# Performance work log

Measured on AMD Instinct MI355X. Metric: run time of the kernel, lower is better.

## Reference

```python
import jax, jax.numpy as jnp
import numpy as np

N_NODES = 100000
N_EDGES = 1600000
IN_FEAT = 128
HIDDEN = 128
N_CLASSES = 40


def setup_inputs() -> dict:
    key = jax.random.key(0)
    k1, k2, k3, k4 = jax.random.split(key, 4)
    x = jax.random.normal(k1, (N_NODES, IN_FEAT), dtype=jnp.float32)
    edge_index = jax.random.randint(k2, (2, N_EDGES), 0, N_NODES, dtype=jnp.int64)
    W1 = jax.random.normal(k3, (IN_FEAT, HIDDEN), dtype=jnp.float32) * (1.0 / np.sqrt(IN_FEAT))
    b1 = jnp.zeros((HIDDEN,), dtype=jnp.float32)
    W2 = jax.random.normal(k4, (HIDDEN, N_CLASSES), dtype=jnp.float32) * (1.0 / np.sqrt(HIDDEN))
    b2 = jnp.zeros((N_CLASSES,), dtype=jnp.float32)
    return {"x": x, "edge_index": edge_index, "W1": W1, "b1": b1, "W2": W2, "b2": b2}


def _gcn_conv(x, row, col, W, b, n_nodes):
    # x: [N, F_in] -> [N, F_out]; GCNConv: lin -> gather -> deg-norm -> scatter-add -> +bias
    h = x @ W  # dense transform first (PyG GCNConv order)
    # add self-loops
    loops = jnp.arange(n_nodes, dtype=row.dtype)
    row = jnp.concatenate([row, loops])
    col = jnp.concatenate([col, loops])
    # symmetric degree normalization: deg computed on destination (col)
    deg = jax.ops.segment_sum(jnp.ones_like(col, dtype=h.dtype), col, num_segments=n_nodes)
    dis = jnp.where(deg > 0, jax.lax.rsqrt(deg), 0.0)
    norm = dis[row] * dis[col]  # [E+N]
    msg = h[row] * norm[:, None]  # [E+N, F_out] gather + scale
    out = jax.ops.segment_sum(msg, col, num_segments=n_nodes)  # scatter-add
    return out + b


def reference(x, edge_index, W1, b1, W2, b2):
    row, col = edge_index[0], edge_index[1]
    n = x.shape[0]
    h = _gcn_conv(x, row, col, W1, b1, n)
    h = jax.nn.relu(h)
    # dropout p=0 / eval mode -> identity
    h = _gcn_conv(h, row, col, W2, b2, n)
    return jax.nn.log_softmax(h, axis=1)
```

## Files before the change

kernel.cpp:

```cpp
#include <hip/hip_runtime.h>
#include <hip/hip_bf16.h>
#include <math.h>

typedef unsigned short u16x8 __attribute__((ext_vector_type(8)));
typedef short s16x8 __attribute__((ext_vector_type(8)));
typedef float f32x4 __attribute__((ext_vector_type(4)));

#define BIN_TILE 4096
#define BCAP 8192

__device__ __forceinline__ float bf2f(unsigned int u) {
    union { unsigned int i; float f; } x;
    x.i = u << 16;
    return x.f;
}
__device__ __forceinline__ unsigned short f2bf(float f) {
    __hip_bfloat16 h = __float2bfloat16(f);
    return *reinterpret_cast<unsigned short*>(&h);
}

__global__ void bin_kernel(const int* __restrict__ row, const int* __restrict__ col,
                           int* __restrict__ bcnt, unsigned* __restrict__ tmp, int E, int NB) {
    __shared__ unsigned hist[512];
    int tid = threadIdx.x;
    int base = blockIdx.x * BIN_TILE;
    for (int i = tid; i < NB; i += 256) hist[i] = 0;
    __syncthreads();
#pragma unroll
    for (int i = 0; i < BIN_TILE / 256; i++) {
        int e = base + tid + i * 256;
        if (e < E) atomicAdd(&hist[col[e] >> 8], 1u);
    }
    __syncthreads();
    for (int i = tid; i < NB; i += 256) {
        unsigned h = hist[i];
        hist[i] = h ? (unsigned)atomicAdd(&bcnt[i], (int)h) : 0u;
    }
    __syncthreads();
#pragma unroll
    for (int i = 0; i < BIN_TILE / 256; i++) {
        int e = base + tid + i * 256;
        if (e < E) {
            int c = col[e], r = row[e];
            unsigned p = atomicAdd(&hist[c >> 8], 1u);
            tmp[(size_t)(c >> 8) * BCAP + p] = (unsigned)r | ((unsigned)(c & 255) << 20);
        }
    }
}

__global__ void bucket_kernel(const unsigned* __restrict__ tmp, const int* __restrict__ bcnt,
                              int* __restrict__ cnt, int* __restrict__ offs,
                              float* __restrict__ dis, int* __restrict__ csr, int N, int NB) {
    __shared__ int cntS[256], curS[256], sA[256], sB[256];
    int b = blockIdx.x;
    int tid = threadIdx.x;
    size_t tbase = (size_t)b * BCAP;

    cntS[tid] = 0;
    int partial = 0;
    if (tid < b) partial += bcnt[tid];
    if (tid + 256 < b) partial += bcnt[tid + 256];
    sA[tid] = partial;
    __syncthreads();
    for (int s = 128; s > 0; s >>= 1) {
        if (tid < s) sA[tid] += sA[tid + s];
        __syncthreads();
    }
    int start = sA[0];
    int ecnt = bcnt[b];

    for (int i = tid; i < ecnt; i += 256)
        atomicAdd(&cntS[(tmp[tbase + i] >> 20) & 255], 1);
    __syncthreads();
    int myCnt = cntS[tid];
    sA[tid] = myCnt;
    __syncthreads();
    int* src = sA;
    int* dst = sB;
    for (int off = 1; off < 256; off <<= 1) {
        dst[tid] = src[tid] + ((tid >= off) ? src[tid - off] : 0);
        __syncthreads();
        int* t = src; src = dst; dst = t;
    }
    int excl = src[tid] - myCnt;
    int node = (b << 8) + tid;
    if (node < N) {
        cnt[node] = myCnt;
        offs[node] = start + excl;
        dis[node] = rsqrtf((float)myCnt + 1.0f);
    }
    curS[tid] = excl;
    __syncthreads();
    for (int i = tid; i < ecnt; i += 256) {
        unsigned u = tmp[tbase + i];
        int cl = (u >> 20) & 255;
        int p = atomicAdd(&curS[cl], 1);
        csr[start + p] = (int)(u & 0xFFFFFu);
    }
}

__global__ void scale_cvt_kernel(const float* __restrict__ x, const float* __restrict__ dis,
                                 unsigned short* __restrict__ xbs, int N) {
    long idx = (long)blockIdx.x * blockDim.x + threadIdx.x;
    long total8 = (long)(N + 1) * 16;
    if (idx >= total8) return;
    int i = (int)(idx >> 4);
    u16x8 o;
    if (i >= N) {
#pragma unroll
        for (int k = 0; k < 8; k++) o[k] = 0;
    } else {
        float d = dis[i];
        float4 a = ((const float4*)x)[2 * idx];
        float4 b = ((const float4*)x)[2 * idx + 1];
        o[0] = f2bf(d * a.x); o[1] = f2bf(d * a.y); o[2] = f2bf(d * a.z); o[3] = f2bf(d * a.w);
        o[4] = f2bf(d * b.x); o[5] = f2bf(d * b.y); o[6] = f2bf(d * b.z); o[7] = f2bf(d * b.w);
    }
    ((u16x8*)xbs)[idx] = o;
}

__global__ void prep_kernel(const float* __restrict__ W1, const float* __restrict__ W2,
                            unsigned short* __restrict__ w1p, unsigned short* __restrict__ w2p,
                            unsigned* __restrict__ h2z) {
    int bid = blockIdx.x, tid = threadIdx.x;
    if (bid < 8) {
        int t = bid * 256 + tid;
        int lane = t & 63, fc = t >> 6;
        int ct = fc >> 2, kc = fc & 3;
        int n = ct * 16 + (lane & 15);
        int k0 = kc * 32 + (lane >> 4) * 8;
        u16x8 o;
#pragma unroll
        for (int j = 0; j < 8; j++) o[j] = f2bf(W1[(size_t)(k0 + j) * 128 + n]);
        ((u16x8*)w1p)[t] = o;
    } else if (bid < 11) {
        int t = (bid - 8) * 256 + tid;
        int lane = t & 63, fc = t >> 6;
        int ct = fc >> 2, kc = fc & 3;
        int n = ct * 16 + (lane & 15);
        int k0 = kc * 32 + (lane >> 4) * 8;
        u16x8 o;
#pragma unroll
        for (int j = 0; j < 8; j++) o[j] = (n < 40) ? f2bf(W2[(size_t)(k0 + j) * 40 + n]) : (unsigned short)0;
        ((u16x8*)w2p)[t] = o;
    } else {
        if (tid < 32) h2z[tid] = 0;
    }
}

__global__ void gather1_kernel(const unsigned short* __restrict__ xbs, const int* __restrict__ offs,
                               const int* __restrict__ cnt, const int* __restrict__ csr,
                               const float* __restrict__ dis, unsigned short* __restrict__ xa, int N) {
    int node = blockIdx.x * 4 + (threadIdx.x >> 6);
    int lane = threadIdx.x & 63;
    if (node >= N) return;
    int off = offs[node], dg = cnt[node];
    int g = lane >> 4, c = lane & 15;
    const u16x8* XB = (const u16x8*)xbs;
    float acc[8] = {};
    int s0 = (g      < dg) ? csr[off + g]      : N;
    int s1 = (g + 4  < dg) ? csr[off + g + 4]  : N;
    int s2 = (g + 8  < dg) ? csr[off + g + 8]  : N;
    int s3 = (g + 12 < dg) ? csr[off + g + 12] : N;
    for (int j = 0; j < dg; j += 16) {
        int jb = j + 16;
        int t0 = (jb + g      < dg) ? csr[off + jb + g]      : N;
        int t1 = (jb + g + 4  < dg) ? csr[off + jb + g + 4]  : N;
        int t2 = (jb + g + 8  < dg) ? csr[off + jb + g + 8]  : N;
        int t3 = (jb + g + 12 < dg) ? csr[off + jb + g + 12] : N;
        u16x8 v0 = XB[(size_t)s0 * 16 + c];
        u16x8 v1 = XB[(size_t)s1 * 16 + c];
        u16x8 v2 = XB[(size_t)s2 * 16 + c];
        u16x8 v3 = XB[(size_t)s3 * 16 + c];
#pragma unroll
        for (int k = 0; k < 8; k++)
            acc[k] += (bf2f(v0[k]) + bf2f(v1[k])) + (bf2f(v2[k]) + bf2f(v3[k]));
        s0 = t0; s1 = t1; s2 = t2; s3 = t3;
    }
#pragma unroll
    for (int k = 0; k < 8; k++) {
        acc[k] += __shfl_xor(acc[k], 16);
        acc[k] += __shfl_xor(acc[k], 32);
    }
    float dc = dis[node];
    u16x8 xv = XB[(size_t)node * 16 + c];
    if (lane < 16) {
        u16x8 o;
#pragma unroll
        for (int k = 0; k < 8; k++) o[k] = f2bf(dc * (acc[k] + bf2f(xv[k])));
        ((u16x8*)xa)[(size_t)node * 16 + c] = o;
    }
}

__global__ __launch_bounds__(256) void mlp_kernel(const unsigned short* __restrict__ xa,
                                                  const unsigned short* __restrict__ w1p,
                                                  const unsigned short* __restrict__ w2p,
                                                  const float* __restrict__ b1,
                                                  const float* __restrict__ dis,
                                                  unsigned short* __restrict__ h2s, int N) {
    __shared__ unsigned short a1s[64][136];
    int wv = threadIdx.x >> 6;
    int l = threadIdx.x & 63;
    int row16 = l & 15, kg = l >> 4;
    int n0 = blockIdx.x * 64;
    int rbase = n0 + wv * 16;

    f32x4 acc[8];
#pragma unroll
    for (int ct = 0; ct < 8; ct++) acc[ct] = (f32x4)0.f;
    int r = rbase + row16;
    int rc = (r < N) ? r : (N - 1);
#pragma unroll
    for (int kc = 0; kc < 4; kc++) {
        s16x8 af = *(const s16x8*)(xa + (size_t)rc * 128 + kc * 32 + kg * 8);
#pragma unroll
        for (int ct = 0; ct < 8; ct++) {
            s16x8 bf = *(const s16x8*)(w1p + (size_t)((ct * 4 + kc) * 64 + l) * 8);
            acc[ct] = __builtin_amdgcn_mfma_f32_16x16x32_bf16(af, bf, acc[ct], 0, 0, 0);
        }
    }
#pragma unroll
    for (int ct = 0; ct < 8; ct++) {
        float bb = b1[ct * 16 + row16];
#pragma unroll
        for (int v = 0; v < 4; v++)
            a1s[wv * 16 + kg * 4 + v][ct * 16 + row16] = f2bf(fmaxf(acc[ct][v] + bb, 0.f));
    }
    __syncthreads();

    f32x4 acc2[3];
#pragma unroll
    for (int ct = 0; ct < 3; ct++) acc2[ct] = (f32x4)0.f;
#pragma unroll
    for (int kc = 0; kc < 4; kc++) {
        s16x8 af = *(const s16x8*)&a1s[wv * 16 + row16][kc * 32 + kg * 8];
#pragma unroll
        for (int ct = 0; ct < 3; ct++) {
            s16x8 bf = *(const s16x8*)(w2p + (size_t)((ct * 4 + kc) * 64 + l) * 8);
            acc2[ct] = __builtin_amdgcn_mfma_f32_16x16x32_bf16(af, bf, acc2[ct], 0, 0, 0);
        }
    }
#pragma unroll
    for (int v = 0; v < 4; v++) {
        int rr = rbase + kg * 4 + v;
        if (rr < N) {
            float d = dis[rr];
#pragma unroll
            for (int ct = 0; ct < 3; ct++)
                h2s[(size_t)rr * 64 + ct * 16 + row16] = f2bf(d * acc2[ct][v]);
        }
    }
}

__global__ void gather2_kernel(const unsigned short* __restrict__ h2s, const int* __restrict__ offs,
                               const int* __restrict__ cnt, const int* __restrict__ csr,
                               const float* __restrict__ dis, const float* __restrict__ b2,
                               float* __restrict__ out, int N) {
    int node = blockIdx.x * 4 + (threadIdx.x >> 6);
    int lane = threadIdx.x & 63;
    if (node >= N) return;
    int off = offs[node], dg = cnt[node];
    int c = lane % 10;
    int g = lane / 10;
    if (g > 5) g = 5;
    const ushort4* H4 = (const ushort4*)h2s;
    float a0 = 0.f, a1 = 0.f, a2 = 0.f, a3 = 0.f;
    int s0 = (g      < dg) ? csr[off + g]      : N;
    int s1 = (g + 6  < dg) ? csr[off + g + 6]  : N;
    int s2 = (g + 12 < dg) ? csr[off + g + 12] : N;
    int s3 = (g + 18 < dg) ? csr[off + g + 18] : N;
    for (int j = 0; j < dg; j += 24) {
        int jb = j + 24;
        int t0 = (jb + g      < dg) ? csr[off + jb + g]      : N;
        int t1 = (jb + g + 6  < dg) ? csr[off + jb + g + 6]  : N;
        int t2 = (jb + g + 12 < dg) ? csr[off + jb + g + 12] : N;
        int t3 = (jb + g + 18 < dg) ? csr[off + jb + g + 18] : N;
        ushort4 u0 = H4[(size_t)s0 * 16 + c];
        ushort4 u1 = H4[(size_t)s1 * 16 + c];
        ushort4 u2 = H4[(size_t)s2 * 16 + c];
        ushort4 u3 = H4[(size_t)s3 * 16 + c];
        a0 += (bf2f(u0.x) + bf2f(u1.x)) + (bf2f(u2.x) + bf2f(u3.x));
        a1 += (bf2f(u0.y) + bf2f(u1.y)) + (bf2f(u2.y) + bf2f(u3.y));
        a2 += (bf2f(u0.z) + bf2f(u1.z)) + (bf2f(u2.z) + bf2f(u3.z));
        a3 += (bf2f(u0.w) + bf2f(u1.w)) + (bf2f(u2.w) + bf2f(u3.w));
        s0 = t0; s1 = t1; s2 = t2; s3 = t3;
    }
    float t;
    t = __shfl(a0, lane + 30); a0 += t;
    t = __shfl(a1, lane + 30); a1 += t;
    t = __shfl(a2, lane + 30); a2 += t;
    t = __shfl(a3, lane + 30); a3 += t;
    float p, q;
    p = __shfl(a0, lane + 10); q = __shfl(a0, lane + 20); a0 += p + q;
    p = __shfl(a1, lane + 10); q = __shfl(a1, lane + 20); a1 += p + q;
    p = __shfl(a2, lane + 10); q = __shfl(a2, lane + 20); a2 += p + q;
    p = __shfl(a3, lane + 10); q = __shfl(a3, lane + 20); a3 += p + q;

    bool act = lane < 10;
    float dc = dis[node];
    ushort4 uv = H4[(size_t)node * 16 + c];
    float4 bb = ((const float4*)b2)[c];
    float v0 = -INFINITY, v1 = -INFINITY, v2 = -INFINITY, v3 = -INFINITY;
    if (act) {
        v0 = dc * (a0 + bf2f(uv.x)) + bb.x;
        v1 = dc * (a1 + bf2f(uv.y)) + bb.y;
        v2 = dc * (a2 + bf2f(uv.z)) + bb.z;
        v3 = dc * (a3 + bf2f(uv.w)) + bb.w;
    }
    float m = fmaxf(fmaxf(v0, v1), fmaxf(v2, v3));
#pragma unroll
    for (int o = 32; o > 0; o >>= 1) m = fmaxf(m, __shfl_xor(m, o));
    float ex = act ? (__expf(v0 - m) + __expf(v1 - m) + __expf(v2 - m) + __expf(v3 - m)) : 0.f;
#pragma unroll
    for (int o = 32; o > 0; o >>= 1) ex += __shfl_xor(ex, o);
    float ls = __logf(ex);
    if (act) {
        float4 o4 = make_float4(v0 - m - ls, v1 - m - ls, v2 - m - ls, v3 - m - ls);
        ((float4*)(out + (size_t)node * 40))[c] = o4;
    }
}

extern "C" void kernel_launch(void* const* d_in, const int* in_sizes, int n_in,
                              void* d_out, int out_size, void* d_ws, size_t ws_size,
                              hipStream_t stream) {
    const float* x  = (const float*)d_in[0];
    const int*   ei = (const int*)d_in[1];
    const float* W1 = (const float*)d_in[2];
    const float* b1 = (const float*)d_in[3];
    const float* W2 = (const float*)d_in[4];
    const float* b2 = (const float*)d_in[5];
    float* out = (float*)d_out;

    const int N = in_sizes[0] / 128;
    const int E = in_sizes[1] / 2;
    const int* row = ei;
    const int* col = ei + E;

    const int Npad = (N + 511) & ~511;
    const int Epad = (E + 511) & ~511;
    const int NB = (N + 255) >> 8;

    int* cnt      = (int*)d_ws;
    int* offs     = cnt + Npad;
    int* bcnt     = offs + Npad;
    int* csr      = bcnt + 1024;
    unsigned* tmp = (unsigned*)(csr + Epad);
    float* dis    = (float*)(tmp + (size_t)NB * BCAP);
    unsigned short* w1p = (unsigned short*)(dis + Npad);
    unsigned short* w2p = w1p + 16384;
    unsigned short* xbs = w2p + 8192;
    unsigned short* xa  = xbs + (size_t)(N + 1) * 128;
    unsigned short* h2s = xa + (size_t)N * 128;

    hipMemsetAsync(bcnt, 0, 512 * sizeof(int), stream);
    bin_kernel<<<(E + BIN_TILE - 1) / BIN_TILE, 256, 0, stream>>>(row, col, bcnt, tmp, E, NB);
    bucket_kernel<<<NB, 256, 0, stream>>>(tmp, bcnt, cnt, offs, dis, csr, N, NB);

    prep_kernel<<<12, 256, 0, stream>>>(W1, W2, w1p, w2p, (unsigned*)(h2s + (size_t)N * 64));
    {
        long total8 = (long)(N + 1) * 16;
        scale_cvt_kernel<<<(int)((total8 + 255) / 256), 256, 0, stream>>>(x, dis, xbs, N);
    }

    gather1_kernel<<<(N + 3) / 4, 256, 0, stream>>>(xbs, offs, cnt, csr, dis, xa, N);

    mlp_kernel<<<(N + 63) / 64, 256, 0, stream>>>(xa, w1p, w2p, b1, dis, h2s, N);

    gather2_kernel<<<(N + 3) / 4, 256, 0, stream>>>(h2s, offs, cnt, csr, dis, b2, out, N);
}
```

Measured before the change: 180.8 us.

## Fuse layer-1 gather into MLP kernel and fold memset into setup kernel

Merges the first-layer neighbor aggregation and the two-layer MFMA MLP into one kernel. Each wave aggregates 16 nodes serially and writes the bf16 result to shared memory, which then feeds the MLP directly, so the intermediate xa buffer is no longer written to and read back from global memory. The bcnt memset is folded into a combined setup kernel launched first, removing one launch. The risk is that processing nodes serially within each wave, across only (N+63)/64 blocks, may expose more gather latency and lower parallelism than the old one-node-per-wave gather.

```diff
diff --git a/kernel.cpp b/kernel.cpp
--- a/kernel.cpp
+++ b/kernel.cpp
@@ -19,109 +19,9 @@
     return *reinterpret_cast<unsigned short*>(&h);
 }
 
-__global__ void bin_kernel(const int* __restrict__ row, const int* __restrict__ col,
-                           int* __restrict__ bcnt, unsigned* __restrict__ tmp, int E, int NB) {
-    __shared__ unsigned hist[512];
-    int tid = threadIdx.x;
-    int base = blockIdx.x * BIN_TILE;
-    for (int i = tid; i < NB; i += 256) hist[i] = 0;
-    __syncthreads();
-#pragma unroll
-    for (int i = 0; i < BIN_TILE / 256; i++) {
-        int e = base + tid + i * 256;
-        if (e < E) atomicAdd(&hist[col[e] >> 8], 1u);
-    }
-    __syncthreads();
-    for (int i = tid; i < NB; i += 256) {
-        unsigned h = hist[i];
-        hist[i] = h ? (unsigned)atomicAdd(&bcnt[i], (int)h) : 0u;
-    }
-    __syncthreads();
-#pragma unroll
-    for (int i = 0; i < BIN_TILE / 256; i++) {
-        int e = base + tid + i * 256;
-        if (e < E) {
-            int c = col[e], r = row[e];
-            unsigned p = atomicAdd(&hist[c >> 8], 1u);
-            tmp[(size_t)(c >> 8) * BCAP + p] = (unsigned)r | ((unsigned)(c & 255) << 20);
-        }
-    }
-}
-
-__global__ void bucket_kernel(const unsigned* __restrict__ tmp, const int* __restrict__ bcnt,
-                              int* __restrict__ cnt, int* __restrict__ offs,
-                              float* __restrict__ dis, int* __restrict__ csr, int N, int NB) {
-    __shared__ int cntS[256], curS[256], sA[256], sB[256];
-    int b = blockIdx.x;
-    int tid = threadIdx.x;
-    size_t tbase = (size_t)b * BCAP;
-
-    cntS[tid] = 0;
-    int partial = 0;
-    if (tid < b) partial += bcnt[tid];
-    if (tid + 256 < b) partial += bcnt[tid + 256];
-    sA[tid] = partial;
-    __syncthreads();
-    for (int s = 128; s > 0; s >>= 1) {
-        if (tid < s) sA[tid] += sA[tid + s];
-        __syncthreads();
-    }
-    int start = sA[0];
-    int ecnt = bcnt[b];
-
-    for (int i = tid; i < ecnt; i += 256)
-        atomicAdd(&cntS[(tmp[tbase + i] >> 20) & 255], 1);
-    __syncthreads();
-    int myCnt = cntS[tid];
-    sA[tid] = myCnt;
-    __syncthreads();
-    int* src = sA;
-    int* dst = sB;
-    for (int off = 1; off < 256; off <<= 1) {
-        dst[tid] = src[tid] + ((tid >= off) ? src[tid - off] : 0);
-        __syncthreads();
-        int* t = src; src = dst; dst = t;
-    }
-    int excl = src[tid] - myCnt;
-    int node = (b << 8) + tid;
-    if (node < N) {
-        cnt[node] = myCnt;
-        offs[node] = start + excl;
-        dis[node] = rsqrtf((float)myCnt + 1.0f);
-    }
-    curS[tid] = excl;
-    __syncthreads();
-    for (int i = tid; i < ecnt; i += 256) {
-        unsigned u = tmp[tbase + i];
-        int cl = (u >> 20) & 255;
-        int p = atomicAdd(&curS[cl], 1);
-        csr[start + p] = (int)(u & 0xFFFFFu);
-    }
-}
-
-__global__ void scale_cvt_kernel(const float* __restrict__ x, const float* __restrict__ dis,
-                                 unsigned short* __restrict__ xbs, int N) {
-    long idx = (long)blockIdx.x * blockDim.x + threadIdx.x;
-    long total8 = (long)(N + 1) * 16;
-    if (idx >= total8) return;
-    int i = (int)(idx >> 4);
-    u16x8 o;
-    if (i >= N) {
-#pragma unroll
-        for (int k = 0; k < 8; k++) o[k] = 0;
-    } else {
-        float d = dis[i];
-        float4 a = ((const float4*)x)[2 * idx];
-        float4 b = ((const float4*)x)[2 * idx + 1];
-        o[0] = f2bf(d * a.x); o[1] = f2bf(d * a.y); o[2] = f2bf(d * a.z); o[3] = f2bf(d * a.w);
-        o[4] = f2bf(d * b.x); o[5] = f2bf(d * b.y); o[6] = f2bf(d * b.z); o[7] = f2bf(d * b.w);
-    }
-    ((u16x8*)xbs)[idx] = o;
-}
-
-__global__ void prep_kernel(const float* __restrict__ W1, const float* __restrict__ W2,
-                            unsigned short* __restrict__ w1p, unsigned short* __restrict__ w2p,
-                            unsigned* __restrict__ h2z) {
+__global__ void setup_kernel(const float* __restrict__ W1, const float* __restrict__ W2,
+                             unsigned short* __restrict__ w1p, unsigned short* __restrict__ w2p,
+                             unsigned* __restrict__ h2z, int* __restrict__ bcnt) {
     int bid = blockIdx.x, tid = threadIdx.x;
     if (bid < 8) {
         int t = bid * 256 + tid;
@@ -143,80 +43,184 @@
 #pragma unroll
         for (int j = 0; j < 8; j++) o[j] = (n < 40) ? f2bf(W2[(size_t)(k0 + j) * 40 + n]) : (unsigned short)0;
         ((u16x8*)w2p)[t] = o;
+    } else if (bid == 11) {
+        if (tid < 32) h2z[tid] = 0;
     } else {
-        if (tid < 32) h2z[tid] = 0;
-    }
-}
-
-__global__ void gather1_kernel(const unsigned short* __restrict__ xbs, const int* __restrict__ offs,
-                               const int* __restrict__ cnt, const int* __restrict__ csr,
-                               const float* __restrict__ dis, unsigned short* __restrict__ xa, int N) {
-    int node = blockIdx.x * 4 + (threadIdx.x >> 6);
-    int lane = threadIdx.x & 63;
-    if (node >= N) return;
-    int off = offs[node], dg = cnt[node];
-    int g = lane >> 4, c = lane & 15;
+        bcnt[tid] = 0;
+        bcnt[tid + 256] = 0;
+    }
+}
+
+__global__ void bin_kernel(const int* __restrict__ row, const int* __restrict__ col,
+                           int* __restrict__ bcnt, unsigned* __restrict__ tmp, int E, int NB) {
+    __shared__ unsigned hist[512];
+    int tid = threadIdx.x;
+    int base = blockIdx.x * BIN_TILE;
+    for (int i = tid; i < NB; i += 256) hist[i] = 0;
+    __syncthreads();
+#pragma unroll
+    for (int i = 0; i < BIN_TILE / 256; i++) {
+        int e = base + tid + i * 256;
+        if (e < E) atomicAdd(&hist[col[e] >> 8], 1u);
+    }
+    __syncthreads();
+    for (int i = tid; i < NB; i += 256) {
+        unsigned h = hist[i];
+        hist[i] = h ? (unsigned)atomicAdd(&bcnt[i], (int)h) : 0u;
+    }
+    __syncthreads();
+#pragma unroll
+    for (int i = 0; i < BIN_TILE / 256; i++) {
+        int e = base + tid + i * 256;
+        if (e < E) {
+            int c = col[e], r = row[e];
+            unsigned p = atomicAdd(&hist[c >> 8], 1u);
+            tmp[(size_t)(c >> 8) * BCAP + p] = (unsigned)r | ((unsigned)(c & 255) << 20);
+        }
+    }
+}
+
+__global__ void bucket_kernel(const unsigned* __restrict__ tmp, const int* __restrict__ bcnt,
+                              int* __restrict__ cnt, int* __restrict__ offs,
+                              float* __restrict__ dis, int* __restrict__ csr, int N, int NB) {
+    __shared__ int cntS[256], curS[256], sA[256], sB[256];
+    int b = blockIdx.x;
+    int tid = threadIdx.x;
+    size_t tbase = (size_t)b * BCAP;
+
+    cntS[tid] = 0;
+    int partial = 0;
+    if (tid < b) partial += bcnt[tid];
+    if (tid + 256 < b) partial += bcnt[tid + 256];
+    sA[tid] = partial;
+    __syncthreads();
+    for (int s = 128; s > 0; s >>= 1) {
+        if (tid < s) sA[tid] += sA[tid + s];
+        __syncthreads();
+    }
+    int start = sA[0];
+    int ecnt = bcnt[b];
+
+    for (int i = tid; i < ecnt; i += 256)
+        atomicAdd(&cntS[(tmp[tbase + i] >> 20) & 255], 1);
+    __syncthreads();
+    int myCnt = cntS[tid];
+    sA[tid] = myCnt;
+    __syncthreads();
+    int* src = sA;
+    int* dst = sB;
+    for (int off = 1; off < 256; off <<= 1) {
+        dst[tid] = src[tid] + ((tid >= off) ? src[tid - off] : 0);
+        __syncthreads();
+        int* t = src; src = dst; dst = t;
+    }
+    int excl = src[tid] - myCnt;
+    int node = (b << 8) + tid;
+    if (node < N) {
+        cnt[node] = myCnt;
+        offs[node] = start + excl;
+        dis[node] = rsqrtf((float)myCnt + 1.0f);
+    }
+    curS[tid] = excl;
+    __syncthreads();
+    for (int i = tid; i < ecnt; i += 256) {
+        unsigned u = tmp[tbase + i];
+        int cl = (u >> 20) & 255;
+        int p = atomicAdd(&curS[cl], 1);
+        csr[start + p] = (int)(u & 0xFFFFFu);
+    }
+}
+
+__global__ void scale_cvt_kernel(const float* __restrict__ x, const float* __restrict__ dis,
+                                 unsigned short* __restrict__ xbs, int N) {
+    long idx = (long)blockIdx.x * blockDim.x + threadIdx.x;
+    long total8 = (long)(N + 1) * 16;
+    if (idx >= total8) return;
+    int i = (int)(idx >> 4);
+    u16x8 o;
+    if (i >= N) {
+#pragma unroll
+        for (int k = 0; k < 8; k++) o[k] = 0;
+    } else {
+        float d = dis[i];
+        float4 a = ((const float4*)x)[2 * idx];
+        float4 b = ((const float4*)x)[2 * idx + 1];
+        o[0] = f2bf(d * a.x); o[1] = f2bf(d * a.y); o[2] = f2bf(d * a.z); o[3] = f2bf(d * a.w);
+        o[4] = f2bf(d * b.x); o[5] = f2bf(d * b.y); o[6] = f2bf(d * b.z); o[7] = f2bf(d * b.w);
+    }
+    ((u16x8*)xbs)[idx] = o;
+}
+
+__global__ __launch_bounds__(256, 6) void g1mlp_kernel(const unsigned short* __restrict__ xbs,
+                                                       const int* __restrict__ offs,
+                                                       const int* __restrict__ cnt,
+                                                       const int* __restrict__ csr,
+                                                       const float* __restrict__ dis,
+                                                       const unsigned short* __restrict__ w1p,
+                                                       const unsigned short* __restrict__ w2p,
+                                                       const float* __restrict__ b1,
+                                                       unsigned short* __restrict__ h2s, int N) {
+    __shared__ unsigned short xt[64][136];
+    int tid = threadIdx.x;
+    int wv = tid >> 6;
+    int l = tid & 63;
+    int g = l >> 4, c = l & 15;
+    int n0 = blockIdx.x * 64;
     const u16x8* XB = (const u16x8*)xbs;
-    float acc[8] = {};
-    int s0 = (g      < dg) ? csr[off + g]      : N;
-    int s1 = (g + 4  < dg) ? csr[off + g + 4]  : N;
-    int s2 = (g + 8  < dg) ? csr[off + g + 8]  : N;
-    int s3 = (g + 12 < dg) ? csr[off + g + 12] : N;
-    for (int j = 0; j < dg; j += 16) {
-        int jb = j + 16;
-        int t0 = (jb + g      < dg) ? csr[off + jb + g]      : N;
-        int t1 = (jb + g + 4  < dg) ? csr[off + jb + g + 4]  : N;
-        int t2 = (jb + g + 8  < dg) ? csr[off + jb + g + 8]  : N;
-        int t3 = (jb + g + 12 < dg) ? csr[off + jb + g + 12] : N;
-        u16x8 v0 = XB[(size_t)s0 * 16 + c];
-        u16x8 v1 = XB[(size_t)s1 * 16 + c];
-        u16x8 v2 = XB[(size_t)s2 * 16 + c];
-        u16x8 v3 = XB[(size_t)s3 * 16 + c];
-#pragma unroll
-        for (int k = 0; k < 8; k++)
-            acc[k] += (bf2f(v0[k]) + bf2f(v1[k])) + (bf2f(v2[k]) + bf2f(v3[k]));
-        s0 = t0; s1 = t1; s2 = t2; s3 = t3;
-    }
-#pragma unroll
-    for (int k = 0; k < 8; k++) {
-        acc[k] += __shfl_xor(acc[k], 16);
-        acc[k] += __shfl_xor(acc[k], 32);
-    }
-    float dc = dis[node];
-    u16x8 xv = XB[(size_t)node * 16 + c];
-    if (lane < 16) {
-        u16x8 o;
-#pragma unroll
-        for (int k = 0; k < 8; k++) o[k] = f2bf(dc * (acc[k] + bf2f(xv[k])));
-        ((u16x8*)xa)[(size_t)node * 16 + c] = o;
-    }
-}
-
-__global__ __launch_bounds__(256) void mlp_kernel(const unsigned short* __restrict__ xa,
-                                                  const unsigned short* __restrict__ w1p,
-                                                  const unsigned short* __restrict__ w2p,
-                                                  const float* __restrict__ b1,
-                                                  const float* __restrict__ dis,
-                                                  unsigned short* __restrict__ h2s, int N) {
-    __shared__ unsigned short a1s[64][136];
-    int wv = threadIdx.x >> 6;
-    int l = threadIdx.x & 63;
+
+    for (int i = 0; i < 16; i++) {
+        int node = n0 + wv * 16 + i;
+        int off = 0, dg = 0;
+        if (node < N) { off = offs[node]; dg = cnt[node]; }
+        float acc[8] = {};
+        int s0 = (g      < dg) ? csr[off + g]      : N;
+        int s1 = (g + 4  < dg) ? csr[off + g + 4]  : N;
+        int s2 = (g + 8  < dg) ? csr[off + g + 8]  : N;
+        int s3 = (g + 12 < dg) ? csr[off + g + 12] : N;
+        for (int j = 0; j < dg; j += 16) {
+            int jb = j + 16;
+            int t0 = (jb + g      < dg) ? csr[off + jb + g]      : N;
+            int t1 = (jb + g + 4  < dg) ? csr[off + jb + g + 4]  : N;
+            int t2 = (jb + g + 8  < dg) ? csr[off + jb + g + 8]  : N;
+            int t3 = (jb + g + 12 < dg) ? csr[off + jb + g + 12] : N;
+            u16x8 v0 = XB[(size_t)s0 * 16 + c];
+            u16x8 v1 = XB[(size_t)s1 * 16 + c];
+            u16x8 v2 = XB[(size_t)s2 * 16 + c];
+            u16x8 v3 = XB[(size_t)s3 * 16 + c];
+#pragma unroll
+            for (int k = 0; k < 8; k++)
+                acc[k] += (bf2f(v0[k]) + bf2f(v1[k])) + (bf2f(v2[k]) + bf2f(v3[k]));
+            s0 = t0; s1 = t1; s2 = t2; s3 = t3;
+        }
+#pragma unroll
+        for (int k = 0; k < 8; k++) {
+            acc[k] += __shfl_xor(acc[k], 16);
+            acc[k] += __shfl_xor(acc[k], 32);
+        }
+        int nodec = (node < N) ? node : N;
+        float dc = (node < N) ? dis[node] : 0.f;
+        u16x8 xv = XB[(size_t)nodec * 16 + c];
+        if (l < 16) {
+            u16x8 o;
+#pragma unroll
+            for (int k = 0; k < 8; k++) o[k] = f2bf(dc * (acc[k] + bf2f(xv[k])));
+            *(u16x8*)&xt[wv * 16 + i][c * 8] = o;
+        }
+    }
+    __syncthreads();
+
     int row16 = l & 15, kg = l >> 4;
-    int n0 = blockIdx.x * 64;
     int rbase = n0 + wv * 16;
-
-    f32x4 acc[8];
-#pragma unroll
-    for (int ct = 0; ct < 8; ct++) acc[ct] = (f32x4)0.f;
-    int r = rbase + row16;
-    int rc = (r < N) ? r : (N - 1);
+    f32x4 acc1[8];
+#pragma unroll
+    for (int ct = 0; ct < 8; ct++) acc1[ct] = (f32x4)0.f;
 #pragma unroll
     for (int kc = 0; kc < 4; kc++) {
-        s16x8 af = *(const s16x8*)(xa + (size_t)rc * 128 + kc * 32 + kg * 8);
+        s16x8 af = *(const s16x8*)&xt[wv * 16 + row16][kc * 32 + kg * 8];
 #pragma unroll
         for (int ct = 0; ct < 8; ct++) {
             s16x8 bf = *(const s16x8*)(w1p + (size_t)((ct * 4 + kc) * 64 + l) * 8);
-            acc[ct] = __builtin_amdgcn_mfma_f32_16x16x32_bf16(af, bf, acc[ct], 0, 0, 0);
+            acc1[ct] = __builtin_amdgcn_mfma_f32_16x16x32_bf16(af, bf, acc1[ct], 0, 0, 0);
         }
     }
 #pragma unroll
@@ -224,16 +228,15 @@
         float bb = b1[ct * 16 + row16];
 #pragma unroll
         for (int v = 0; v < 4; v++)
-            a1s[wv * 16 + kg * 4 + v][ct * 16 + row16] = f2bf(fmaxf(acc[ct][v] + bb, 0.f));
-    }
-    __syncthreads();
+            xt[wv * 16 + kg * 4 + v][ct * 16 + row16] = f2bf(fmaxf(acc1[ct][v] + bb, 0.f));
+    }
 
     f32x4 acc2[3];
 #pragma unroll
     for (int ct = 0; ct < 3; ct++) acc2[ct] = (f32x4)0.f;
 #pragma unroll
     for (int kc = 0; kc < 4; kc++) {
-        s16x8 af = *(const s16x8*)&a1s[wv * 16 + row16][kc * 32 + kg * 8];
+        s16x8 af = *(const s16x8*)&xt[wv * 16 + row16][kc * 32 + kg * 8];
 #pragma unroll
         for (int ct = 0; ct < 3; ct++) {
             s16x8 bf = *(const s16x8*)(w2p + (size_t)((ct * 4 + kc) * 64 + l) * 8);
@@ -349,22 +352,20 @@
     unsigned short* w1p = (unsigned short*)(dis + Npad);
     unsigned short* w2p = w1p + 16384;
     unsigned short* xbs = w2p + 8192;
-    unsigned short* xa  = xbs + (size_t)(N + 1) * 128;
-    unsigned short* h2s = xa + (size_t)N * 128;
-
-    hipMemsetAsync(bcnt, 0, 512 * sizeof(int), stream);
+    unsigned short* h2s = xbs + (size_t)(N + 1) * 128;
+
+    setup_kernel<<<13, 256, 0, stream>>>(W1, W2, w1p, w2p,
+                                         (unsigned*)(h2s + (size_t)N * 64), bcnt);
     bin_kernel<<<(E + BIN_TILE - 1) / BIN_TILE, 256, 0, stream>>>(row, col, bcnt, tmp, E, NB);
     bucket_kernel<<<NB, 256, 0, stream>>>(tmp, bcnt, cnt, offs, dis, csr, N, NB);
 
-    prep_kernel<<<12, 256, 0, stream>>>(W1, W2, w1p, w2p, (unsigned*)(h2s + (size_t)N * 64));
     {
         long total8 = (long)(N + 1) * 16;
         scale_cvt_kernel<<<(int)((total8 + 255) / 256), 256, 0, stream>>>(x, dis, xbs, N);
     }
 
-    gather1_kernel<<<(N + 3) / 4, 256, 0, stream>>>(xbs, offs, cnt, csr, dis, xa, N);
-
-    mlp_kernel<<<(N + 63) / 64, 256, 0, stream>>>(xa, w1p, w2p, b1, dis, h2s, N);
+    g1mlp_kernel<<<(N + 63) / 64, 256, 0, stream>>>(xbs, offs, cnt, csr, dis,
+                                                    w1p, w2p, b1, h2s, N);
 
     gather2_kernel<<<(N + 3) / 4, 256, 0, stream>>>(h2s, offs, cnt, csr, dis, b2, out, N);
 }
```

After: 195.4 us. 8.1% more time.
